# Kernel tuning notes

Hardware: AMD Instinct MI355X
Metric: run time of the kernel (lower is better)

Reference implementation:

```python
import jax, jax.numpy as jnp
import numpy as np


@jax.custom_vjp
def sign_ste(x):
    return jnp.sign(x)

def _sign_ste_fwd(x):
    return jnp.sign(x), x

def _sign_ste_bwd(x, g):
    gate = (jnp.abs(x) < 1.0).astype(g.dtype)
    return (g * gate,)

sign_ste.defvjp(_sign_ste_fwd, _sign_ste_bwd)


def setup_inputs() -> dict:
    key = jax.random.key(0)
    ks = jax.random.split(key, 6)
    B, S, D_IN, D_OUT, R = 4, 4096, 4096, 4096, 128
    x = jax.random.normal(ks[0], (B, S, D_IN), dtype=jnp.float32)
    U_latent = jax.random.normal(ks[1], (D_OUT, R), dtype=jnp.float32) * 0.05
    V_latent = jax.random.normal(ks[2], (D_IN, R), dtype=jnp.float32) * 0.05
    s1 = jax.random.uniform(ks[3], (D_OUT,), dtype=jnp.float32, minval=0.01, maxval=0.1)
    s2 = jax.random.uniform(ks[4], (D_IN,), dtype=jnp.float32, minval=0.01, maxval=0.1)
    bias = jax.random.normal(ks[5], (D_OUT,), dtype=jnp.float32) * 0.02
    return {"x": x, "U_latent": U_latent, "V_latent": V_latent, "s1": s1, "s2": s2, "bias": bias}


def reference(x, U_latent, V_latent, s1, s2, bias):
    cdtype = x.dtype
    U_sign = sign_ste(U_latent.astype(cdtype))  # [d_out, r]
    V_sign = sign_ste(V_latent.astype(cdtype))  # [d_in, r]
    z = x * s2.astype(cdtype)                   # [..., d_in]
    z = z @ V_sign                               # [..., r]
    z = z @ U_sign.T                             # [..., d_out]
    z = z * s1.astype(cdtype)
    z = z + bias.astype(cdtype)
    return z
```

## Files before the change

### kernel.cpp

```cpp
#include <hip/hip_runtime.h>

typedef float f32x4 __attribute__((ext_vector_type(4)));
typedef _Float16 f16x8 __attribute__((ext_vector_type(8)));
typedef __fp16 fp16x2 __attribute__((ext_vector_type(2)));

#define M_TOT 16384
#define K_IN  4096
#define R_DIM 128
#define N_OUT 4096

__device__ __forceinline__ _Float16 sign_f16(float v) {
  return v > 0.f ? (_Float16)1.f : (v < 0.f ? (_Float16)-1.f : (_Float16)0.f);
}

__device__ __forceinline__ void cvt8v(f32x4 a, f32x4 b, f16x8& h, f16x8& l) {
#pragma unroll
  for (int j = 0; j < 2; ++j) {
    fp16x2 h0 = __builtin_amdgcn_cvt_pkrtz(a[2 * j], a[2 * j + 1]);
    fp16x2 h1 = __builtin_amdgcn_cvt_pkrtz(b[2 * j], b[2 * j + 1]);
    fp16x2 l0 = __builtin_amdgcn_cvt_pkrtz(a[2 * j] - (float)h0[0], a[2 * j + 1] - (float)h0[1]);
    fp16x2 l1 = __builtin_amdgcn_cvt_pkrtz(b[2 * j] - (float)h1[0], b[2 * j + 1] - (float)h1[1]);
    h[2 * j] = (_Float16)h0[0]; h[2 * j + 1] = (_Float16)h0[1];
    h[4 + 2 * j] = (_Float16)h1[0]; h[5 + 2 * j] = (_Float16)h1[1];
    l[2 * j] = (_Float16)l0[0]; l[2 * j + 1] = (_Float16)l0[1];
    l[4 + 2 * j] = (_Float16)l1[0]; l[5 + 2 * j] = (_Float16)l1[1];
  }
}

__device__ __forceinline__ void gload16(const void* g, void* l) {
  __builtin_amdgcn_global_load_lds((const __attribute__((address_space(1))) unsigned int*)g,
                                   (__attribute__((address_space(3))) unsigned int*)l, 16, 0, 0);
}

__global__ __launch_bounds__(256)
void k_prep(const float* __restrict__ U, const float* __restrict__ V,
            _Float16* __restrict__ VsT_sw, _Float16* __restrict__ Us) {
  __shared__ _Float16 tl[128 * 72];
  const int t = threadIdx.x;
  const int b = blockIdx.x;

  {
    size_t base = (size_t)b * 2048 + (size_t)t * 8;
    f32x4 u0 = *(const f32x4*)(U + base);
    f32x4 u1 = *(const f32x4*)(U + base + 4);
    f16x8 s;
#pragma unroll
    for (int j = 0; j < 4; ++j) { s[j] = sign_f16(u0[j]); s[j + 4] = sign_f16(u1[j]); }
    *(f16x8*)(Us + base) = s;
  }

  if (b < 64) {
#pragma unroll
    for (int it = 0; it < 8; ++it) {
      int idx4 = it * 256 + t;
      int kl = idx4 >> 5;
      int r4 = (idx4 & 31) * 4;
      f32x4 v = *(const f32x4*)(V + (size_t)(b * 64 + kl) * R_DIM + r4);
#pragma unroll
      for (int j = 0; j < 4; ++j) tl[(r4 + j) * 72 + kl] = sign_f16(v[j]);
    }
    __syncthreads();
#pragma unroll
    for (int c = 0; c < 4; ++c) {
      int off = t * 64 + c * 16;
      int r = off >> 7;
      int cB = (off & 127) ^ ((r & 7) << 4);
      f16x8 o = *(const f16x8*)(tl + r * 72 + (cB >> 1));
      *(f16x8*)((char*)VsT_sw + (size_t)b * 16384 + off) = o;
    }
  }
}

__global__ __launch_bounds__(256, 3)
void k1_z(const float* __restrict__ x, const float* __restrict__ s2,
          const _Float16* __restrict__ VsT_sw,
          _Float16* __restrict__ Zswh, _Float16* __restrict__ Zswl) {
  __shared__ char smem[49152];
  const int t = threadIdx.x;
  const int lane = t & 63;
  const int wave = t >> 6;
  const int m0 = blockIdx.x * 32;

  const int srow = t >> 3;
  const int scol = (t & 7) * 8;
  const float* xrow = x + (size_t)(m0 + srow) * K_IN + scol;
  const int aoff = srow * 128 + (((t & 7) * 16) ^ ((srow & 7) << 4));

  const int wr = wave & 1, wc = wave >> 1;
  const int arow = wr * 16 + (lane & 15);
  const int abyte = arow * 128;
  const int asw = (arow & 7) << 4;
  const int kq16 = (lane >> 4) * 16;
  int brow[4], bsw[4];
#pragma unroll
  for (int nf = 0; nf < 4; ++nf) {
    brow[nf] = wc * 64 + nf * 16 + (lane & 15);
    bsw[nf] = (brow[nf] & 7) << 4;
  }

  f32x4 acc[4];
#pragma unroll
  for (int i = 0; i < 4; ++i) acc[i] = (f32x4){0.f, 0.f, 0.f, 0.f};

  {
    f32x4 a = *(const f32x4*)xrow;
    f32x4 bql = *(const f32x4*)(xrow + 4);
    f32x4 sa = *(const f32x4*)(s2 + scol);
    f32x4 sb = *(const f32x4*)(s2 + scol + 4);
    f16x8 h, l;
    cvt8v(a * sa, bql * sb, h, l);
    *(f16x8*)(smem + aoff) = h;
    *(f16x8*)(smem + 4096 + aoff) = l;
#pragma unroll
    for (int q = 0; q < 4; ++q)
      gload16((const char*)VsT_sw + (size_t)wave * 1024 + q * 4096 + lane * 16,
              smem + 16384 + wave * 1024 + q * 4096);
  }
  __syncthreads();

  f32x4 xn0 = *(const f32x4*)(xrow + 64);
  f32x4 xn1 = *(const f32x4*)(xrow + 68);
  f32x4 sn0 = *(const f32x4*)(s2 + 64 + scol);
  f32x4 sn1 = *(const f32x4*)(s2 + 64 + scol + 4);

  for (int kt = 0; kt < 64; ++kt) {
    const int cur = kt & 1, nxt = cur ^ 1;
    if (kt < 63) {
#pragma unroll
      for (int q = 0; q < 4; ++q)
        gload16((const char*)VsT_sw + (size_t)(kt + 1) * 16384 + wave * 1024 + q * 4096 + lane * 16,
                smem + 16384 + nxt * 16384 + wave * 1024 + q * 4096);
      f16x8 h, l;
      cvt8v(xn0 * sn0, xn1 * sn1, h, l);
      *(f16x8*)(smem + nxt * 8192 + aoff) = h;
      *(f16x8*)(smem + nxt * 8192 + 4096 + aoff) = l;
      if (kt < 62) {
        xn0 = *(const f32x4*)(xrow + (kt + 2) * 64);
        xn1 = *(const f32x4*)(xrow + (kt + 2) * 64 + 4);
        sn0 = *(const f32x4*)(s2 + (kt + 2) * 64 + scol);
        sn1 = *(const f32x4*)(s2 + (kt + 2) * 64 + scol + 4);
      }
    }
#pragma unroll
    for (int kk = 0; kk < 2; ++kk) {
      const int cb = kk * 64 + kq16;
      f16x8 ah = *(const f16x8*)(smem + cur * 8192 + abyte + (cb ^ asw));
      f16x8 al = *(const f16x8*)(smem + cur * 8192 + 4096 + abyte + (cb ^ asw));
#pragma unroll
      for (int nf = 0; nf < 4; ++nf) {
        f16x8 bfv = *(const f16x8*)(smem + 16384 + cur * 16384 + brow[nf] * 128 + (cb ^ bsw[nf]));
        acc[nf] = __builtin_amdgcn_mfma_f32_16x16x32_f16(ah, bfv, acc[nf], 0, 0, 0);
        acc[nf] = __builtin_amdgcn_mfma_f32_16x16x32_f16(al, bfv, acc[nf], 0, 0, 0);
      }
    }
    __syncthreads();
  }

  float* ZT = (float*)smem;
#pragma unroll
  for (int nf = 0; nf < 4; ++nf)
#pragma unroll
    for (int j = 0; j < 4; ++j)
      ZT[(wr * 16 + (lane >> 4) * 4 + j) * 132 + wc * 64 + nf * 16 + (lane & 15)] = acc[nf][j];
  __syncthreads();
  {
    const int lr = t >> 3;
    const int c0 = (t & 7) * 16;
    f32x4 v0 = *(const f32x4*)(ZT + lr * 132 + c0);
    f32x4 v1 = *(const f32x4*)(ZT + lr * 132 + c0 + 4);
    f32x4 v2 = *(const f32x4*)(ZT + lr * 132 + c0 + 8);
    f32x4 v3 = *(const f32x4*)(ZT + lr * 132 + c0 + 12);
    f16x8 h0, l0, h1, l1;
    cvt8v(v0, v1, h0, l0);
    cvt8v(v2, v3, h1, l1);
    const int m = m0 + lr;
    const int sw = (lr & 7) << 4;
    char* ph = (char*)Zswh + (size_t)m * 256;
    char* pl = (char*)Zswl + (size_t)m * 256;
    *(f16x8*)(ph + ((c0 * 2) ^ sw)) = h0;
    *(f16x8*)(ph + ((c0 * 2 + 16) ^ sw)) = h1;
    *(f16x8*)(pl + ((c0 * 2) ^ sw)) = l0;
    *(f16x8*)(pl + ((c0 * 2 + 16) ^ sw)) = l1;
  }
}

__global__ __launch_bounds__(256, 4)
void k2_out(const _Float16* __restrict__ Zswh, const _Float16* __restrict__ Zswl,
            const _Float16* __restrict__ Us, const float* __restrict__ s1,
            const float* __restrict__ bias, float* __restrict__ out) {
  __shared__ char smem[32768];
  const int t = threadIdx.x;
  const int lane = t & 63;
  const int wave = t >> 6;
  const int bid = blockIdx.x;
  const int nb = bid & 31;
  const int mb = bid >> 5;
  const int m0 = mb * 64, n0 = nb * 128;
  const int wm = wave & 1, wn = wave >> 1;

  f16x8 bf[4][4];
#pragma unroll
  for (int ks = 0; ks < 4; ++ks)
#pragma unroll
    for (int nf = 0; nf < 4; ++nf) {
      const int n = n0 + wn * 64 + nf * 16 + (lane & 15);
      bf[ks][nf] = *(const f16x8*)(Us + (size_t)n * R_DIM + ks * 32 + (lane >> 4) * 8);
    }

  const char* gh = (const char*)Zswh + (size_t)m0 * 256;
  const char* gl = (const char*)Zswl + (size_t)m0 * 256;
#pragma unroll
  for (int q = 0; q < 4; ++q) {
    gload16(gh + wave * 1024 + q * 4096 + lane * 16, smem + wave * 1024 + q * 4096);
    gload16(gl + wave * 1024 + q * 4096 + lane * 16, smem + 16384 + wave * 1024 + q * 4096);
  }
  __syncthreads();

  f32x4 acc[2][4] = {};
  const int kq = (lane >> 4) * 16;
#pragma unroll
  for (int mf = 0; mf < 2; ++mf) {
    const int lr = wm * 32 + mf * 16 + (lane & 15);
    const int sw = (lr & 7) << 4;
#pragma unroll
    for (int ks = 0; ks < 4; ++ks) {
      const int cb = (ks * 64 + kq) ^ sw;
      f16x8 ah = *(const f16x8*)(smem + lr * 256 + cb);
      f16x8 al = *(const f16x8*)(smem + 16384 + lr * 256 + cb);
#pragma unroll
      for (int nf = 0; nf < 4; ++nf) {
        acc[mf][nf] = __builtin_amdgcn_mfma_f32_16x16x32_f16(ah, bf[ks][nf], acc[mf][nf], 0, 0, 0);
        acc[mf][nf] = __builtin_amdgcn_mfma_f32_16x16x32_f16(al, bf[ks][nf], acc[mf][nf], 0, 0, 0);
      }
    }
  }

#pragma unroll
  for (int nf = 0; nf < 4; ++nf) {
    const int col = n0 + wn * 64 + nf * 16 + (lane & 15);
    const float sv = s1[col];
    const float bv = bias[col];
#pragma unroll
    for (int mf = 0; mf < 2; ++mf) {
      const int row = m0 + wm * 32 + mf * 16 + (lane >> 4) * 4;
#pragma unroll
      for (int j = 0; j < 4; ++j)
        out[(size_t)(row + j) * N_OUT + col] = acc[mf][nf][j] * sv + bv;
    }
  }
}

extern "C" void kernel_launch(void* const* d_in, const int* in_sizes, int n_in,
                              void* d_out, int out_size, void* d_ws, size_t ws_size,
                              hipStream_t stream) {
  const float* x    = (const float*)d_in[0];
  const float* U    = (const float*)d_in[1];
  const float* V    = (const float*)d_in[2];
  const float* s1   = (const float*)d_in[3];
  const float* s2   = (const float*)d_in[4];
  const float* bias = (const float*)d_in[5];
  float* out = (float*)d_out;

  char* w = (char*)d_ws;
  _Float16* VsT_sw = (_Float16*)(w);
  _Float16* Us     = (_Float16*)(w + (1 << 20));
  _Float16* Zswh   = (_Float16*)(w + (2 << 20));
  _Float16* Zswl   = (_Float16*)(w + (6 << 20));

  k_prep<<<dim3(256), dim3(256), 0, stream>>>(U, V, VsT_sw, Us);
  k1_z<<<dim3(512), dim3(256), 0, stream>>>(x, s2, VsT_sw, Zswh, Zswl);
  k2_out<<<dim3(8192), dim3(256), 0, stream>>>(Zswh, Zswl, Us, s1, bias, out);
}
```

Measured before the change: 524.5 us.

## Load x fragments directly into registers and widen k1 block to 8 waves

The first GEMM kernel no longer stages the scaled x tile through shared memory. Each lane now loads its MFMA A-fragment straight from global memory, converts it to hi/lo fp16 in registers, and double-buffers the next tile with a manually ping-ponged register set. The block grows from 4 to 8 waves, each computing 32 output columns instead of 64, and shared memory drops to 32KB holding only the sign(V) tiles. This removes LDS writes and reads for A and raises wave count, at the cost of redundant A conversion across column waves and less coalesced x loads (32-byte chunks per row).

```diff
diff --git a/kernel.cpp b/kernel.cpp
--- a/kernel.cpp
+++ b/kernel.cpp
@@ -71,116 +71,109 @@
   }
 }
 
-__global__ __launch_bounds__(256, 3)
+#define LOADX(T, X0, X1, X2, X3, S0, S1, S2, S3)            \
+  {                                                          \
+    X0 = *(const f32x4*)(xp + (T) * 64);                     \
+    X1 = *(const f32x4*)(xp + (T) * 64 + 4);                 \
+    X2 = *(const f32x4*)(xp + (T) * 64 + 32);                \
+    X3 = *(const f32x4*)(xp + (T) * 64 + 36);                \
+    S0 = *(const f32x4*)(sp + (T) * 64);                     \
+    S1 = *(const f32x4*)(sp + (T) * 64 + 4);                 \
+    S2 = *(const f32x4*)(sp + (T) * 64 + 32);                \
+    S3 = *(const f32x4*)(sp + (T) * 64 + 36);                \
+  }
+
+#define K1BODY(T, X0, X1, X2, X3, S0, S1, S2, S3, Y0, Y1, Y2, Y3, R0, R1, R2, R3) \
+  {                                                                                \
+    f16x8 ah0, al0, ah1, al1;                                                      \
+    cvt8v(X0 * S0, X1 * S1, ah0, al0);                                             \
+    cvt8v(X2 * S2, X3 * S3, ah1, al1);                                             \
+    if ((T) < 63) {                                                                \
+      const char* src = (const char*)VsT_sw + (size_t)((T) + 1) * 16384 +          \
+                        wave * 1024 + lane * 16;                                   \
+      char* dst = smem + (((T) + 1) & 1) * 16384 + wave * 1024;                    \
+      gload16(src, dst);                                                           \
+      gload16(src + 8192, dst + 8192);                                             \
+      LOADX((T) + 1, Y0, Y1, Y2, Y3, R0, R1, R2, R3);                              \
+    }                                                                              \
+    const char* bb = smem + ((T) & 1) * 16384;                                     \
+    f16x8 b00 = *(const f16x8*)(bb + brow0 * 128 + ((kq16) ^ bsw0));               \
+    f16x8 b01 = *(const f16x8*)(bb + brow0 * 128 + ((64 + kq16) ^ bsw0));          \
+    f16x8 b10 = *(const f16x8*)(bb + brow1 * 128 + ((kq16) ^ bsw1));               \
+    f16x8 b11 = *(const f16x8*)(bb + brow1 * 128 + ((64 + kq16) ^ bsw1));          \
+    acc0 = __builtin_amdgcn_mfma_f32_16x16x32_f16(ah0, b00, acc0, 0, 0, 0);        \
+    acc0 = __builtin_amdgcn_mfma_f32_16x16x32_f16(al0, b00, acc0, 0, 0, 0);        \
+    acc0 = __builtin_amdgcn_mfma_f32_16x16x32_f16(ah1, b01, acc0, 0, 0, 0);        \
+    acc0 = __builtin_amdgcn_mfma_f32_16x16x32_f16(al1, b01, acc0, 0, 0, 0);        \
+    acc1 = __builtin_amdgcn_mfma_f32_16x16x32_f16(ah0, b10, acc1, 0, 0, 0);        \
+    acc1 = __builtin_amdgcn_mfma_f32_16x16x32_f16(al0, b10, acc1, 0, 0, 0);        \
+    acc1 = __builtin_amdgcn_mfma_f32_16x16x32_f16(ah1, b11, acc1, 0, 0, 0);        \
+    acc1 = __builtin_amdgcn_mfma_f32_16x16x32_f16(al1, b11, acc1, 0, 0, 0);        \
+    __syncthreads();                                                               \
+  }
+
+__global__ __launch_bounds__(512, 4)
 void k1_z(const float* __restrict__ x, const float* __restrict__ s2,
           const _Float16* __restrict__ VsT_sw,
           _Float16* __restrict__ Zswh, _Float16* __restrict__ Zswl) {
-  __shared__ char smem[49152];
+  __shared__ char smem[32768];
   const int t = threadIdx.x;
   const int lane = t & 63;
   const int wave = t >> 6;
   const int m0 = blockIdx.x * 32;
-
-  const int srow = t >> 3;
-  const int scol = (t & 7) * 8;
-  const float* xrow = x + (size_t)(m0 + srow) * K_IN + scol;
-  const int aoff = srow * 128 + (((t & 7) * 16) ^ ((srow & 7) << 4));
-
   const int wr = wave & 1, wc = wave >> 1;
-  const int arow = wr * 16 + (lane & 15);
-  const int abyte = arow * 128;
-  const int asw = (arow & 7) << 4;
+
+  const int kq8 = (lane >> 4) * 8;
   const int kq16 = (lane >> 4) * 16;
-  int brow[4], bsw[4];
-#pragma unroll
-  for (int nf = 0; nf < 4; ++nf) {
-    brow[nf] = wc * 64 + nf * 16 + (lane & 15);
-    bsw[nf] = (brow[nf] & 7) << 4;
-  }
-
-  f32x4 acc[4];
-#pragma unroll
-  for (int i = 0; i < 4; ++i) acc[i] = (f32x4){0.f, 0.f, 0.f, 0.f};
+  const int arow = m0 + wr * 16 + (lane & 15);
+  const float* xp = x + (size_t)arow * K_IN + kq8;
+  const float* sp = s2 + kq8;
+
+  const int brow0 = wc * 32 + (lane & 15);
+  const int brow1 = brow0 + 16;
+  const int bsw0 = (brow0 & 7) << 4;
+  const int bsw1 = (brow1 & 7) << 4;
+
+  f32x4 acc0 = {0.f, 0.f, 0.f, 0.f};
+  f32x4 acc1 = {0.f, 0.f, 0.f, 0.f};
 
   {
-    f32x4 a = *(const f32x4*)xrow;
-    f32x4 bql = *(const f32x4*)(xrow + 4);
-    f32x4 sa = *(const f32x4*)(s2 + scol);
-    f32x4 sb = *(const f32x4*)(s2 + scol + 4);
-    f16x8 h, l;
-    cvt8v(a * sa, bql * sb, h, l);
-    *(f16x8*)(smem + aoff) = h;
-    *(f16x8*)(smem + 4096 + aoff) = l;
-#pragma unroll
-    for (int q = 0; q < 4; ++q)
-      gload16((const char*)VsT_sw + (size_t)wave * 1024 + q * 4096 + lane * 16,
-              smem + 16384 + wave * 1024 + q * 4096);
-  }
+    const char* src = (const char*)VsT_sw + wave * 1024 + lane * 16;
+    char* dst = smem + wave * 1024;
+    gload16(src, dst);
+    gload16(src + 8192, dst + 8192);
+  }
+  f32x4 xa0, xa1, xa2, xa3, sa0, sa1, sa2, sa3;
+  f32x4 xb0, xb1, xb2, xb3, sb0, sb1, sb2, sb3;
+  LOADX(0, xa0, xa1, xa2, xa3, sa0, sa1, sa2, sa3);
   __syncthreads();
 
-  f32x4 xn0 = *(const f32x4*)(xrow + 64);
-  f32x4 xn1 = *(const f32x4*)(xrow + 68);
-  f32x4 sn0 = *(const f32x4*)(s2 + 64 + scol);
-  f32x4 sn1 = *(const f32x4*)(s2 + 64 + scol + 4);
-
-  for (int kt = 0; kt < 64; ++kt) {
-    const int cur = kt & 1, nxt = cur ^ 1;
-    if (kt < 63) {
-#pragma unroll
-      for (int q = 0; q < 4; ++q)
-        gload16((const char*)VsT_sw + (size_t)(kt + 1) * 16384 + wave * 1024 + q * 4096 + lane * 16,
-                smem + 16384 + nxt * 16384 + wave * 1024 + q * 4096);
-      f16x8 h, l;
-      cvt8v(xn0 * sn0, xn1 * sn1, h, l);
-      *(f16x8*)(smem + nxt * 8192 + aoff) = h;
-      *(f16x8*)(smem + nxt * 8192 + 4096 + aoff) = l;
-      if (kt < 62) {
-        xn0 = *(const f32x4*)(xrow + (kt + 2) * 64);
-        xn1 = *(const f32x4*)(xrow + (kt + 2) * 64 + 4);
-        sn0 = *(const f32x4*)(s2 + (kt + 2) * 64 + scol);
-        sn1 = *(const f32x4*)(s2 + (kt + 2) * 64 + scol + 4);
-      }
-    }
-#pragma unroll
-    for (int kk = 0; kk < 2; ++kk) {
-      const int cb = kk * 64 + kq16;
-      f16x8 ah = *(const f16x8*)(smem + cur * 8192 + abyte + (cb ^ asw));
-      f16x8 al = *(const f16x8*)(smem + cur * 8192 + 4096 + abyte + (cb ^ asw));
-#pragma unroll
-      for (int nf = 0; nf < 4; ++nf) {
-        f16x8 bfv = *(const f16x8*)(smem + 16384 + cur * 16384 + brow[nf] * 128 + (cb ^ bsw[nf]));
-        acc[nf] = __builtin_amdgcn_mfma_f32_16x16x32_f16(ah, bfv, acc[nf], 0, 0, 0);
-        acc[nf] = __builtin_amdgcn_mfma_f32_16x16x32_f16(al, bfv, acc[nf], 0, 0, 0);
-      }
-    }
-    __syncthreads();
+  for (int tt = 0; tt < 32; ++tt) {
+    const int t0 = tt * 2;
+    K1BODY(t0,     xa0, xa1, xa2, xa3, sa0, sa1, sa2, sa3,
+                   xb0, xb1, xb2, xb3, sb0, sb1, sb2, sb3);
+    K1BODY(t0 + 1, xb0, xb1, xb2, xb3, sb0, sb1, sb2, sb3,
+                   xa0, xa1, xa2, xa3, sa0, sa1, sa2, sa3);
   }
 
   float* ZT = (float*)smem;
 #pragma unroll
-  for (int nf = 0; nf < 4; ++nf)
-#pragma unroll
-    for (int j = 0; j < 4; ++j)
-      ZT[(wr * 16 + (lane >> 4) * 4 + j) * 132 + wc * 64 + nf * 16 + (lane & 15)] = acc[nf][j];
+  for (int j = 0; j < 4; ++j) {
+    ZT[(wr * 16 + (lane >> 4) * 4 + j) * 132 + wc * 32 + (lane & 15)]      = acc0[j];
+    ZT[(wr * 16 + (lane >> 4) * 4 + j) * 132 + wc * 32 + 16 + (lane & 15)] = acc1[j];
+  }
   __syncthreads();
   {
-    const int lr = t >> 3;
-    const int c0 = (t & 7) * 16;
+    const int lr = t >> 4;
+    const int c0 = (t & 15) * 8;
     f32x4 v0 = *(const f32x4*)(ZT + lr * 132 + c0);
     f32x4 v1 = *(const f32x4*)(ZT + lr * 132 + c0 + 4);
-    f32x4 v2 = *(const f32x4*)(ZT + lr * 132 + c0 + 8);
-    f32x4 v3 = *(const f32x4*)(ZT + lr * 132 + c0 + 12);
-    f16x8 h0, l0, h1, l1;
-    cvt8v(v0, v1, h0, l0);
-    cvt8v(v2, v3, h1, l1);
+    f16x8 h, l;
+    cvt8v(v0, v1, h, l);
+    const int sw = (lr & 7) << 4;
     const int m = m0 + lr;
-    const int sw = (lr & 7) << 4;
-    char* ph = (char*)Zswh + (size_t)m * 256;
-    char* pl = (char*)Zswl + (size_t)m * 256;
-    *(f16x8*)(ph + ((c0 * 2) ^ sw)) = h0;
-    *(f16x8*)(ph + ((c0 * 2 + 16) ^ sw)) = h1;
-    *(f16x8*)(pl + ((c0 * 2) ^ sw)) = l0;
-    *(f16x8*)(pl + ((c0 * 2 + 16) ^ sw)) = l1;
+    *(f16x8*)((char*)Zswh + (size_t)m * 256 + ((c0 * 2) ^ sw)) = h;
+    *(f16x8*)((char*)Zswl + (size_t)m * 256 + ((c0 * 2) ^ sw)) = l;
   }
 }
 
@@ -268,6 +261,6 @@
   _Float16* Zswl   = (_Float16*)(w + (6 << 20));
 
   k_prep<<<dim3(256), dim3(256), 0, stream>>>(U, V, VsT_sw, Us);
-  k1_z<<<dim3(512), dim3(256), 0, stream>>>(x, s2, VsT_sw, Zswh, Zswl);
+  k1_z<<<dim3(512), dim3(512), 0, stream>>>(x, s2, VsT_sw, Zswh, Zswl);
   k2_out<<<dim3(8192), dim3(256), 0, stream>>>(Zswh, Zswl, Us, s1, bias, out);
 }
```

Measured after the change: 607.4 us. 15.8% more time.
